# Optimization experiments

Hardware: AMD Instinct MI355X
Metric: run time of the kernel (lower is better)

## Reference

```python
import jax, jax.numpy as jnp
import numpy as np

N = 200000
EPS = 1e-6

def _build_indices():
    # irreps = 128x0e + 64x1e + 32x2e, mirroring MySeperableLayerNorm.__init__ bookkeeping
    scalar_idx = np.arange(128)                       # positions of 0e scalars
    scalar_ch = np.arange(128)                        # their channel ids
    vector_idx = np.arange(128, 480)                  # positions of vector components
    vector_ch_local = np.concatenate([
        np.repeat(np.arange(64), 3),
        np.repeat(np.arange(64, 96), 5),
    ])
    ch_expand = np.concatenate([
        np.arange(128),                               # scalar channels 0..127
        np.repeat(np.arange(128, 192), 3),            # 1e channels 128..191
        np.repeat(np.arange(192, 224), 5),            # 2e channels 192..223
    ])
    return scalar_idx, scalar_ch, vector_idx, vector_ch_local, ch_expand

def setup_inputs() -> dict:
    key = jax.random.key(0)
    ks = jax.random.split(key, 8)
    si, sc, vi, vcl, ce = _build_indices()
    f32 = jnp.float32
    inp = {
        "x": jax.random.normal(ks[0], (N, 480), dtype=f32),
        "W1": jax.random.normal(ks[1], (56, 224), dtype=f32) * 0.05,
        "b1": jax.random.normal(ks[2], (56,), dtype=f32) * 0.05,
        "W2": jax.random.normal(ks[3], (224, 56), dtype=f32) * 0.05,
        "b2": jax.random.normal(ks[4], (224,), dtype=f32) * 0.05,
        "aff_w": 1.0 + 0.1 * jax.random.normal(ks[5], (1, 224), dtype=f32),
        "aff_b": 0.1 * jax.random.normal(ks[6], (1, 128), dtype=f32),
        "scalar_idx": jnp.asarray(si, jnp.int32),
        "scalar_ch": jnp.asarray(sc, jnp.int32),
        "vector_idx": jnp.asarray(vi, jnp.int32),
        "vector_ch_local": jnp.asarray(vcl, jnp.int32),
        "ch_expand": jnp.asarray(ce, jnp.int32),
    }
    return inp

def reference(x, W1, b1, W2, b2, aff_w, aff_b,
              scalar_idx, scalar_ch, vector_idx, vector_ch_local, ch_expand):
    n = x.shape[0]
    num_features = W2.shape[0]
    num_scalar = scalar_idx.shape[0]
    num_vector = num_features - num_scalar

    # --- invariants ---
    scalars = x[:, scalar_idx]                                   # [N, S]
    scalars_centered = scalars - scalars.mean(axis=1, keepdims=True)
    vec_sq = x[:, vector_idx] ** 2                               # [N, Vdim]
    # scatter_mean over vector components -> per-vector mean square
    sums = jnp.zeros((n, num_vector), x.dtype).at[:, vector_ch_local].add(vec_sq)
    counts = jnp.zeros((num_vector,), x.dtype).at[vector_ch_local].add(1.0)
    vectors_rms = jnp.sqrt(sums / counts + EPS)                  # [N, V]

    feats = jnp.concatenate([scalars_centered, vectors_rms], axis=1)  # [N, S+V]
    # gate_norm == 'rms'
    feats = feats * jax.lax.rsqrt(jnp.mean(feats ** 2, axis=1, keepdims=True) + EPS)

    # --- gating MLP (Linear -> SiLU -> Linear) ---
    h = jax.nn.silu(feats @ W1.T + b1)                           # [N, H]
    gate = jax.nn.sigmoid(h @ W2.T + b2) * aff_w                 # [N, C]

    # --- scatter-affine expansion ---
    x_out = x * gate[:, ch_expand]                               # [N, D]
    x_out = x_out.at[:, scalar_idx].set(scalars_centered * gate[:, scalar_ch] + aff_b)
    return x_out
```

## Files before the change

kernel.cpp:

```cpp
#include <hip/hip_runtime.h>

typedef __bf16 bf16;
typedef bf16 bf16x8 __attribute__((ext_vector_type(8)));
typedef float f32x4 __attribute__((ext_vector_type(4)));

#define EPS 1e-6f


__global__ __launch_bounds__(256) void fused(
    const float* __restrict__ x,
    const float* __restrict__ b1v, const float* __restrict__ b2v,
    const float* __restrict__ aw,  const float* __restrict__ ab,
    const bf16* __restrict__ W1b,  const bf16* __restrict__ W2b,
    float* __restrict__ out)
{
    __shared__ unsigned char smem[4 * 14688];
    const int tid = threadIdx.x;
    const int wv  = tid >> 6;
    const int l   = tid & 63;
    const int q   = l >> 4;
    const int c   = l & 15;
    unsigned char* reg = smem + wv * 14688;
    bf16*  feats = (bf16*)reg;
    float* vx    = (float*)(reg + 7424);
    bf16*  Hs    = (bf16*)(reg + 7424);
    bf16*  gateb = (bf16*)(reg + 7424);
    float* srow  = (float*)(reg + 14624);
    const int r0 = blockIdx.x * 64 + wv * 16;

    for (int i = 0; i < 16; ++i) {
        const float* xr = x + (r0 + i) * 480;
        f32x4 a0 = *(const f32x4*)(xr + 4 * l);
        f32x4 a1 = {};
        if (l < 56) a1 = *(const f32x4*)(xr + 256 + 4 * l);
        *(f32x4*)(vx + 4 * l) = a0;
        if (l < 56) *(f32x4*)(vx + 256 + 4 * l) = a1;
        __syncthreads();

        float v0 = vx[l], v1 = vx[64 + l];
        float su = v0 + v1;
        #pragma unroll
        for (int m = 1; m < 64; m <<= 1) su += __shfl_xor(su, m);
        const float mean = su * (1.0f / 128.0f);
        const float c0 = v0 - mean, c1 = v1 - mean;

        const float t0 = vx[128 + 3 * l], t1 = vx[129 + 3 * l], t2 = vx[130 + 3 * l];
        const float ra = sqrtf((t0 * t0 + t1 * t1 + t2 * t2) * (1.0f / 3.0f) + EPS);
        float rb = 0.0f;
        if (l < 32) {
            const float* p = vx + 320 + 5 * l;
            float g5 = p[0]*p[0] + p[1]*p[1] + p[2]*p[2] + p[3]*p[3] + p[4]*p[4];
            rb = sqrtf(g5 * 0.2f + EPS);
        }

        bf16* fr = feats + i * 232;
        fr[l]        = (bf16)c0;
        fr[64 + l]   = (bf16)c1;
        fr[128 + l]  = (bf16)ra;
        if (l < 32) fr[192 + l] = (bf16)rb;

        float ms = c0 * c0 + c1 * c1 + ra * ra + rb * rb;
        #pragma unroll
        for (int m = 1; m < 64; m <<= 1) ms += __shfl_xor(ms, m);
        if (l == 0) srow[i] = rsqrtf(ms * (1.0f / 224.0f) + EPS);
        __syncthreads();
    }

    bf16x8 af[7];
    {
        const bf16* frow = feats + c * 232;
        #pragma unroll
        for (int ks = 0; ks < 7; ++ks)
            af[ks] = *(const bf16x8*)(frow + ks * 32 + q * 8);
    }
    #pragma unroll
    for (int t = 0; t < 4; ++t) {
        f32x4 acc = {0.f, 0.f, 0.f, 0.f};
        const int n = t * 16 + c;
        const bf16* wrow = W1b + n * 224 + q * 8;
        #pragma unroll
        for (int ks = 0; ks < 7; ++ks)
            acc = __builtin_amdgcn_mfma_f32_16x16x32_bf16(
                      af[ks], *(const bf16x8*)(wrow + ks * 32), acc, 0, 0, 0);
        float bb = 0.f;
        if (n < 56) bb = b1v[n];
        #pragma unroll
        for (int r = 0; r < 4; ++r) {
            const int row = q * 4 + r;
            const float z = acc[r] * srow[row] + bb;
            float hv = 0.f;
            if (n < 56) hv = z / (1.f + __expf(-z));
            Hs[row * 72 + n] = (bf16)hv;
        }
    }
    __syncthreads();

    const bf16x8 ha0 = *(const bf16x8*)(Hs + c * 72 + q * 8);
    const bf16x8 ha1 = *(const bf16x8*)(Hs + c * 72 + 32 + q * 8);
    __syncthreads();
    for (int t = 0; t < 14; ++t) {
        f32x4 acc = {0.f, 0.f, 0.f, 0.f};
        const int nn = t * 16 + c;
        const bf16* wrow = W2b + nn * 64 + q * 8;
        acc = __builtin_amdgcn_mfma_f32_16x16x32_bf16(ha0, *(const bf16x8*)(wrow),      acc, 0, 0, 0);
        acc = __builtin_amdgcn_mfma_f32_16x16x32_bf16(ha1, *(const bf16x8*)(wrow + 32), acc, 0, 0, 0);
        const float bb = b2v[nn];
        const float a  = aw[nn];
        #pragma unroll
        for (int r = 0; r < 4; ++r) {
            const int row = q * 4 + r;
            const float g = a / (1.f + __expf(-(acc[r] + bb)));
            gateb[row * 225 + nn] = (bf16)g;
        }
    }
    __syncthreads();

    for (int i = 0; i < 16; ++i) {
        const int base = (r0 + i) * 480;
        const bf16* fr = feats + i * 232;
        const bf16* gr = gateb + i * 225;
        const float cen0 = (float)fr[l];
        const float cen1 = (float)fr[64 + l];
        out[base + l]      = cen0 * (float)gr[l]      + ab[l];
        out[base + 64 + l] = cen1 * (float)gr[64 + l] + ab[64 + l];
        #pragma unroll
        for (int k = 0; k < 6; ++k) {
            const int cc = 128 + 64 * k + l;
            if (cc < 480) {
                const int d  = cc - 128;
                const int ch = (d < 192) ? (128 + d / 3) : (192 + (d - 192) / 5);
                out[base + cc] = x[base + cc] * (float)gr[ch];
            }
        }
    }
}

__global__ __launch_bounds__(256) void convert_w(
    const float* __restrict__ W1, const float* __restrict__ W2,
    bf16* __restrict__ W1b, bf16* __restrict__ W2b)
{
    const int t = blockIdx.x * 256 + threadIdx.x;
    if (t < 64 * 224) {
        const int n = t / 224, k = t % 224;
        W1b[t] = (n < 56) ? (bf16)W1[n * 224 + k] : (bf16)0.f;
    } else {
        const int u = t - 64 * 224;
        const int n = u >> 6, kk = u & 63;
        W2b[u] = (kk < 56) ? (bf16)W2[n * 56 + kk] : (bf16)0.f;
    }
}

extern "C" void kernel_launch(void* const* d_in, const int* in_sizes, int n_in,
                              void* d_out, int out_size, void* d_ws, size_t ws_size,
                              hipStream_t stream) {
    const float* x  = (const float*)d_in[0];
    const float* W1 = (const float*)d_in[1];
    const float* b1 = (const float*)d_in[2];
    const float* W2 = (const float*)d_in[3];
    const float* b2 = (const float*)d_in[4];
    const float* aw = (const float*)d_in[5];
    const float* ab = (const float*)d_in[6];
    bf16* W1b = (bf16*)d_ws;
    bf16* W2b = W1b + 64 * 224;
    const int rows = in_sizes[0] / 480;
    convert_w<<<112, 256, 0, stream>>>(W1, W2, W1b, W2b);
    fused<<<rows / 64, 256, 0, stream>>>(x, b1, b2, aw, ab, W1b, W2b, (float*)d_out);
}
```

Baseline: 862.4 us.

## Load rows into registers, use wave barriers, and halve per-wave shared memory

```diff
diff --git a/kernel.cpp b/kernel.cpp
--- a/kernel.cpp
+++ b/kernel.cpp
@@ -7,64 +7,73 @@
 #define EPS 1e-6f
 
 
-__global__ __launch_bounds__(256) void fused(
+__global__ __launch_bounds__(256, 4) void fused(
     const float* __restrict__ x,
     const float* __restrict__ b1v, const float* __restrict__ b2v,
     const float* __restrict__ aw,  const float* __restrict__ ab,
     const bf16* __restrict__ W1b,  const bf16* __restrict__ W2b,
     float* __restrict__ out)
 {
-    __shared__ unsigned char smem[4 * 14688];
+    __shared__ unsigned char smem[4 * 7488];
     const int tid = threadIdx.x;
     const int wv  = tid >> 6;
     const int l   = tid & 63;
     const int q   = l >> 4;
     const int c   = l & 15;
-    unsigned char* reg = smem + wv * 14688;
+    unsigned char* reg = smem + wv * 7488;
     bf16*  feats = (bf16*)reg;
-    float* vx    = (float*)(reg + 7424);
-    bf16*  Hs    = (bf16*)(reg + 7424);
-    bf16*  gateb = (bf16*)(reg + 7424);
-    float* srow  = (float*)(reg + 14624);
+    bf16*  Hs    = (bf16*)reg;
+    bf16*  gateb = (bf16*)reg;
+    float* srow  = (float*)(reg + 7424);
     const int r0 = blockIdx.x * 64 + wv * 16;
 
-    for (int i = 0; i < 16; ++i) {
-        const float* xr = x + (r0 + i) * 480;
-        f32x4 a0 = *(const f32x4*)(xr + 4 * l);
-        f32x4 a1 = {};
-        if (l < 56) a1 = *(const f32x4*)(xr + 256 + 4 * l);
-        *(f32x4*)(vx + 4 * l) = a0;
-        if (l < 56) *(f32x4*)(vx + 256 + 4 * l) = a1;
-        __syncthreads();
+    float cen0[16], cen1[16];
+    #pragma unroll
+    for (int b = 0; b < 4; ++b) {
+        float v0[4], v1[4], t0[4], t1[4], t2[4], p0[4], p1[4], p2[4], p3[4], p4[4];
+        #pragma unroll
+        for (int j = 0; j < 4; ++j) {
+            const float* xr = x + (r0 + 4 * b + j) * 480;
+            v0[j] = xr[l];
+            v1[j] = xr[64 + l];
+            t0[j] = xr[128 + 3 * l];
+            t1[j] = xr[129 + 3 * l];
+            t2[j] = xr[130 + 3 * l];
+            if (l < 32) {
+                const float* pp = xr + 320 + 5 * l;
+                p0[j] = pp[0]; p1[j] = pp[1]; p2[j] = pp[2]; p3[j] = pp[3]; p4[j] = pp[4];
+            }
+        }
+        #pragma unroll
+        for (int j = 0; j < 4; ++j) {
+            const int i = 4 * b + j;
+            float su = v0[j] + v1[j];
+            #pragma unroll
+            for (int m = 1; m < 64; m <<= 1) su += __shfl_xor(su, m);
+            const float mean = su * (1.0f / 128.0f);
+            const float c0 = v0[j] - mean, c1 = v1[j] - mean;
+            cen0[i] = c0; cen1[i] = c1;
 
-        float v0 = vx[l], v1 = vx[64 + l];
-        float su = v0 + v1;
-        #pragma unroll
-        for (int m = 1; m < 64; m <<= 1) su += __shfl_xor(su, m);
-        const float mean = su * (1.0f / 128.0f);
-        const float c0 = v0 - mean, c1 = v1 - mean;
+            const float ra = sqrtf((t0[j]*t0[j] + t1[j]*t1[j] + t2[j]*t2[j]) * (1.0f / 3.0f) + EPS);
+            float rb = 0.0f;
+            if (l < 32) {
+                const float g5 = p0[j]*p0[j] + p1[j]*p1[j] + p2[j]*p2[j] + p3[j]*p3[j] + p4[j]*p4[j];
+                rb = sqrtf(g5 * 0.2f + EPS);
+            }
 
-        const float t0 = vx[128 + 3 * l], t1 = vx[129 + 3 * l], t2 = vx[130 + 3 * l];
-        const float ra = sqrtf((t0 * t0 + t1 * t1 + t2 * t2) * (1.0f / 3.0f) + EPS);
-        float rb = 0.0f;
-        if (l < 32) {
-            const float* p = vx + 320 + 5 * l;
-            float g5 = p[0]*p[0] + p[1]*p[1] + p[2]*p[2] + p[3]*p[3] + p[4]*p[4];
-            rb = sqrtf(g5 * 0.2f + EPS);
+            bf16* fr = feats + i * 232;
+            fr[l]       = (bf16)c0;
+            fr[64 + l]  = (bf16)c1;
+            fr[128 + l] = (bf16)ra;
+            if (l < 32) fr[192 + l] = (bf16)rb;
+
+            float ms = c0 * c0 + c1 * c1 + ra * ra + rb * rb;
+            #pragma unroll
+            for (int m = 1; m < 64; m <<= 1) ms += __shfl_xor(ms, m);
+            if (l == 0) srow[i] = rsqrtf(ms * (1.0f / 224.0f) + EPS);
         }
-
-        bf16* fr = feats + i * 232;
-        fr[l]        = (bf16)c0;
-        fr[64 + l]   = (bf16)c1;
-        fr[128 + l]  = (bf16)ra;
-        if (l < 32) fr[192 + l] = (bf16)rb;
-
-        float ms = c0 * c0 + c1 * c1 + ra * ra + rb * rb;
-        #pragma unroll
-        for (int m = 1; m < 64; m <<= 1) ms += __shfl_xor(ms, m);
-        if (l == 0) srow[i] = rsqrtf(ms * (1.0f / 224.0f) + EPS);
-        __syncthreads();
     }
+    __builtin_amdgcn_wave_barrier();
 
     bf16x8 af[7];
     {
@@ -73,6 +82,7 @@
         for (int ks = 0; ks < 7; ++ks)
             af[ks] = *(const bf16x8*)(frow + ks * 32 + q * 8);
     }
+    __builtin_amdgcn_wave_barrier();
     #pragma unroll
     for (int t = 0; t < 4; ++t) {
         f32x4 acc = {0.f, 0.f, 0.f, 0.f};
@@ -93,11 +103,12 @@
             Hs[row * 72 + n] = (bf16)hv;
         }
     }
-    __syncthreads();
+    __builtin_amdgcn_wave_barrier();
 
     const bf16x8 ha0 = *(const bf16x8*)(Hs + c * 72 + q * 8);
     const bf16x8 ha1 = *(const bf16x8*)(Hs + c * 72 + 32 + q * 8);
-    __syncthreads();
+    __builtin_amdgcn_wave_barrier();
+    #pragma unroll
     for (int t = 0; t < 14; ++t) {
         f32x4 acc = {0.f, 0.f, 0.f, 0.f};
         const int nn = t * 16 + c;
@@ -113,16 +124,15 @@
             gateb[row * 225 + nn] = (bf16)g;
         }
     }
-    __syncthreads();
+    __builtin_amdgcn_wave_barrier();
 
+    const float ab0 = ab[l], ab1 = ab[64 + l];
+    #pragma unroll
     for (int i = 0; i < 16; ++i) {
         const int base = (r0 + i) * 480;
-        const bf16* fr = feats + i * 232;
         const bf16* gr = gateb + i * 225;
-        const float cen0 = (float)fr[l];
-        const float cen1 = (float)fr[64 + l];
-        out[base + l]      = cen0 * (float)gr[l]      + ab[l];
-        out[base + 64 + l] = cen1 * (float)gr[64 + l] + ab[64 + l];
+        out[base + l]      = cen0[i] * (float)gr[l]      + ab0;
+        out[base + 64 + l] = cen1[i] * (float)gr[64 + l] + ab1;
         #pragma unroll
         for (int k = 0; k < 6; ++k) {
             const int cc = 128 + 64 * k + l;
```

Result: faster. 791.1 us (-8.3%).
